# Kernel optimization log

Measured on AMD Instinct MI355X. Metric: run time of the kernel, lower is better.

The kernel has to match this reference:

```python
import jax, jax.numpy as jnp
import numpy as np

B, C, T = 512, 256, 256
E, K, G = 8, 5, 8
EPS = 1e-5


def setup_inputs() -> dict:
    key = jax.random.key(0)
    k1, k2, k3, k4 = jax.random.split(key, 4)
    x = jax.random.normal(k1, (B, C, T), dtype=jnp.float32)
    use_expert_i = jax.random.randint(k2, (B,), 0, E, dtype=jnp.int32)
    # per-expert Conv1d params: weight [E, Cout, Cin, K], bias [E, Cout]
    W = jax.random.normal(k3, (E, C, C, K), dtype=jnp.float32) * 0.05
    b = jax.random.normal(k4, (E, C), dtype=jnp.float32) * 0.05
    # per-expert GroupNorm affine params (torch default init: gamma=1, beta=0)
    gamma = jnp.ones((E, C), dtype=jnp.float32)
    beta = jnp.zeros((E, C), dtype=jnp.float32)
    return {"x": x, "use_expert_i": use_expert_i, "W": W, "b": b,
            "gamma": gamma, "beta": beta}


def _mish(y):
    return y * jnp.tanh(jax.nn.softplus(y))


def reference(x, use_expert_i, W, b, gamma, beta):
    # Top-1 one-hot routing => weight is exactly 1 for the selected expert, so
    # output[b] = Mish(GroupNorm(Conv1d_{e_b}(x[b]))). Gather per-sample params
    # instead of looping over experts (same math, vectorized).
    pad = K // 2
    Wb = W[use_expert_i]        # [B, Cout, Cin, K]
    bb = b[use_expert_i]        # [B, Cout]
    gb = gamma[use_expert_i]    # [B, Cout]
    betab = beta[use_expert_i]  # [B, Cout]

    def per_sample_conv(xi, wi, bi):
        # xi: [Cin, T], wi: [Cout, Cin, K] -> [Cout, T] ('same' padding)
        y = jax.lax.conv_general_dilated(xi[None], wi, window_strides=(1,),
                                         padding=[(pad, pad)])[0]
        return y + bi[:, None]

    y = jax.vmap(per_sample_conv)(x, Wb, bb)  # [B, C, T]

    # GroupNorm: normalize over (channels-in-group, length) per sample
    yg = y.reshape(B, G, C // G, T)
    mu = jnp.mean(yg, axis=(2, 3), keepdims=True)
    var = jnp.var(yg, axis=(2, 3), keepdims=True)
    yn = ((yg - mu) * jax.lax.rsqrt(var + EPS)).reshape(B, C, T)
    yn = yn * gb[:, :, None] + betab[:, :, None]
    return _mish(yn)
```

## Files before the change

### kernel.cpp

```cpp
#include <hip/hip_runtime.h>
#include <cmath>

constexpr int Bn = 512, Cn = 256, Tn = 256, En = 8;
constexpr float EPSf = 1e-5f;

using bf16x8 = __attribute__((ext_vector_type(8))) short;
using f32x4  = __attribute__((ext_vector_type(4))) float;

__device__ __forceinline__ ushort f2bf(float f) {
    uint u = __builtin_bit_cast(uint, f);
    uint r = u + 0x7FFFu + ((u >> 16) & 1u);
    return (ushort)(r >> 16);
}

__global__ __launch_bounds__(256)
void wconv_kernel(const float* __restrict__ Wf, ushort* __restrict__ Wws) {
    int idx = blockIdx.x * 256 + threadIdx.x;
    int ci = idx & 255, co = (idx >> 8) & 255, e = idx >> 16;
    const float* src = Wf + (size_t)idx * 5;
#pragma unroll
    for (int k = 0; k < 5; ++k)
        Wws[(((size_t)(e * 5 + k) * 256 + co) << 8) + ci] = f2bf(src[k]);
}

template<bool USE_WS>
__global__ __launch_bounds__(256)
void conv_mfma(const float* __restrict__ x, const int* __restrict__ expert,
               const float* __restrict__ Wf, const ushort* __restrict__ Wws,
               const float* __restrict__ bias, const float* __restrict__ gamma,
               const float* __restrict__ beta, float* __restrict__ out) {
    int id = blockIdx.x;
    int wg = (id & 7) * 256 + (id >> 3);
    int b  = wg >> 2;
    int gp = wg & 3;
    int e  = __builtin_amdgcn_readfirstlane(expert[b]);
    const int cb = gp * 64;

    const int tid = threadIdx.x;
    const int w = tid >> 6, l = tid & 63, q = l >> 4, r = l & 15;

    __shared__ ushort xT[260 * 40];
    __shared__ float red[4][4];

    f32x4 acc[4][4];
#pragma unroll
    for (int m = 0; m < 4; ++m)
#pragma unroll
        for (int n = 0; n < 4; ++n) acc[m][n] = f32x4{0.f, 0.f, 0.f, 0.f};

    if (tid < 4) {
        int row = (tid < 2) ? tid : (256 + tid);
#pragma unroll
        for (int i = 0; i < 10; ++i)
            *reinterpret_cast<uint2*>(&xT[row * 40 + i * 4]) = make_uint2(0u, 0u);
    }

    for (int ci0 = 0; ci0 < Cn; ci0 += 32) {
        __syncthreads();
        const float* xb = x + ((size_t)b * Cn + ci0 + w * 8) * Tn;
#pragma unroll
        for (int tt = 0; tt < 4; ++tt) {
            const int t = tt * 64 + l;
            float v[8];
#pragma unroll
            for (int rr = 0; rr < 8; ++rr) v[rr] = xb[rr * Tn + t];
            uint p0 = (uint)f2bf(v[0]) | ((uint)f2bf(v[1]) << 16);
            uint p1 = (uint)f2bf(v[2]) | ((uint)f2bf(v[3]) << 16);
            uint p2 = (uint)f2bf(v[4]) | ((uint)f2bf(v[5]) << 16);
            uint p3 = (uint)f2bf(v[6]) | ((uint)f2bf(v[7]) << 16);
            *reinterpret_cast<uint2*>(&xT[(t + 2) * 40 + w * 8])     = make_uint2(p0, p1);
            *reinterpret_cast<uint2*>(&xT[(t + 2) * 40 + w * 8 + 4]) = make_uint2(p2, p3);
        }
        __syncthreads();

#pragma unroll
        for (int k = 0; k < 5; ++k) {
            bf16x8 A[4];
#pragma unroll
            for (int m = 0; m < 4; ++m) {
                if (USE_WS) {
                    A[m] = *reinterpret_cast<const bf16x8*>(
                        Wws + (((size_t)((e * 5 + k) * 256 + cb + m * 16 + r)) << 8)
                            + ci0 + q * 8);
                } else {
                    bf16x8 a;
#pragma unroll
                    for (int j = 0; j < 8; ++j)
                        a[j] = (short)f2bf(
                            Wf[((size_t)((e * 256 + cb + m * 16 + r)) * 256
                                + ci0 + q * 8 + j) * 5 + k]);
                    A[m] = a;
                }
            }
#pragma unroll
            for (int n = 0; n < 4; ++n) {
                const bf16x8 Bf = *reinterpret_cast<const bf16x8*>(
                    &xT[(w * 64 + n * 16 + r + k) * 40 + q * 8]);
#pragma unroll
                for (int m = 0; m < 4; ++m)
                    acc[m][n] = __builtin_amdgcn_mfma_f32_16x16x32_bf16(
                        A[m], Bf, acc[m][n], 0, 0, 0);
            }
        }
    }

    float s1a = 0.f, s2a = 0.f, s1b = 0.f, s2b = 0.f;
#pragma unroll
    for (int m = 0; m < 4; ++m) {
#pragma unroll
        for (int i = 0; i < 4; ++i) {
            const float bv = bias[e * 256 + cb + m * 16 + q * 4 + i];
#pragma unroll
            for (int n = 0; n < 4; ++n) {
                const float v = acc[m][n][i] + bv;
                acc[m][n][i] = v;
                if (m < 2) { s1a += v; s2a += v * v; }
                else       { s1b += v; s2b += v * v; }
            }
        }
    }
#pragma unroll
    for (int off = 32; off; off >>= 1) {
        s1a += __shfl_xor(s1a, off); s2a += __shfl_xor(s2a, off);
        s1b += __shfl_xor(s1b, off); s2b += __shfl_xor(s2b, off);
    }
    if (l == 0) { red[w][0] = s1a; red[w][1] = s2a; red[w][2] = s1b; red[w][3] = s2b; }
    __syncthreads();
    const float S1a = red[0][0] + red[1][0] + red[2][0] + red[3][0];
    const float S2a = red[0][1] + red[1][1] + red[2][1] + red[3][1];
    const float S1b = red[0][2] + red[1][2] + red[2][2] + red[3][2];
    const float S2b = red[0][3] + red[1][3] + red[2][3] + red[3][3];

    constexpr float invn = 1.0f / (32 * 256);
    const float mua = S1a * invn, mub = S1b * invn;
    const float rsa = rsqrtf(fmaf(-mua, mua, S2a * invn) + EPSf);
    const float rsb = rsqrtf(fmaf(-mub, mub, S2b * invn) + EPSf);

#pragma unroll
    for (int m = 0; m < 4; ++m) {
        const float mu = (m < 2) ? mua : mub;
        const float rs = (m < 2) ? rsa : rsb;
#pragma unroll
        for (int i = 0; i < 4; ++i) {
            const int co = cb + m * 16 + q * 4 + i;
            const float sc = gamma[e * 256 + co] * rs;
            const float sh = beta[e * 256 + co] - mu * sc;
            float* orow = out + ((size_t)(b * 256 + co)) * 256 + w * 64 + r;
#pragma unroll
            for (int n = 0; n < 4; ++n) {
                const float y = fmaf(acc[m][n][i], sc, sh);
                const float u  = __expf(y);
                const float t2 = u * (u + 2.f);
                const float ms = (y > 20.f) ? y : y * t2 / (t2 + 2.f);
                orow[n * 16] = ms;
            }
        }
    }
}

extern "C" void kernel_launch(void* const* d_in, const int* in_sizes, int n_in,
                              void* d_out, int out_size, void* d_ws, size_t ws_size,
                              hipStream_t stream) {
    const float* x      = (const float*)d_in[0];
    const int*   expert = (const int*)  d_in[1];
    const float* Wf     = (const float*)d_in[2];
    const float* bias   = (const float*)d_in[3];
    const float* gamma  = (const float*)d_in[4];
    const float* beta   = (const float*)d_in[5];
    float* out = (float*)d_out;

    const size_t W_BYTES = (size_t)En * 5 * 256 * 256 * 2;
    if (ws_size >= W_BYTES) {
        ushort* Wws = (ushort*)d_ws;
        hipLaunchKernelGGL(wconv_kernel, dim3(2048), dim3(256), 0, stream, Wf, Wws);
        hipLaunchKernelGGL((conv_mfma<true>), dim3(2048), dim3(256), 0, stream,
                           x, expert, Wf, Wws, bias, gamma, beta, out);
    } else {
        hipLaunchKernelGGL((conv_mfma<false>), dim3(2048), dim3(256), 0, stream,
                           x, expert, Wf, nullptr, bias, gamma, beta, out);
    }
}
```

Before: 228.3 us.

## Process one full sample per block with 512 threads and prefetched x staging

Each block now computes all 256 output channels for one sample with 8 waves arranged 4x2, instead of four blocks per sample each doing 64 channels. This means the input tile is loaded and converted to bf16 once per sample rather than four times. The next input chunk's global loads are issued into registers before the current chunk's MFMAs, then written to LDS after a barrier, so load latency overlaps compute. In exchange, accumulators double to 128 floats per thread, which raises register pressure under the 512-thread launch bound, and the grid shrinks to 512 blocks.

```diff
diff --git a/kernel.cpp b/kernel.cpp
--- a/kernel.cpp
+++ b/kernel.cpp
@@ -24,29 +24,26 @@
 }
 
 template<bool USE_WS>
-__global__ __launch_bounds__(256)
+__global__ __launch_bounds__(512, 2)
 void conv_mfma(const float* __restrict__ x, const int* __restrict__ expert,
                const float* __restrict__ Wf, const ushort* __restrict__ Wws,
                const float* __restrict__ bias, const float* __restrict__ gamma,
                const float* __restrict__ beta, float* __restrict__ out) {
-    int id = blockIdx.x;
-    int wg = (id & 7) * 256 + (id >> 3);
-    int b  = wg >> 2;
-    int gp = wg & 3;
-    int e  = __builtin_amdgcn_readfirstlane(expert[b]);
-    const int cb = gp * 64;
+    const int b = blockIdx.x;
+    const int e = __builtin_amdgcn_readfirstlane(expert[b]);
 
     const int tid = threadIdx.x;
     const int w = tid >> 6, l = tid & 63, q = l >> 4, r = l & 15;
+    const int wm = w >> 1, wn = w & 1;
 
     __shared__ ushort xT[260 * 40];
-    __shared__ float red[4][4];
+    __shared__ float red[8][4];
 
-    f32x4 acc[4][4];
+    f32x4 acc[4][8];
 #pragma unroll
     for (int m = 0; m < 4; ++m)
 #pragma unroll
-        for (int n = 0; n < 4; ++n) acc[m][n] = f32x4{0.f, 0.f, 0.f, 0.f};
+        for (int n = 0; n < 8; ++n) acc[m][n] = f32x4{0.f, 0.f, 0.f, 0.f};
 
     if (tid < 4) {
         int row = (tid < 2) ? tid : (256 + tid);
@@ -55,23 +52,37 @@
             *reinterpret_cast<uint2*>(&xT[row * 40 + i * 4]) = make_uint2(0u, 0u);
     }
 
-    for (int ci0 = 0; ci0 < Cn; ci0 += 32) {
-        __syncthreads();
-        const float* xb = x + ((size_t)b * Cn + ci0 + w * 8) * Tn;
-#pragma unroll
-        for (int tt = 0; tt < 4; ++tt) {
-            const int t = tt * 64 + l;
-            float v[8];
-#pragma unroll
-            for (int rr = 0; rr < 8; ++rr) v[rr] = xb[rr * Tn + t];
-            uint p0 = (uint)f2bf(v[0]) | ((uint)f2bf(v[1]) << 16);
-            uint p1 = (uint)f2bf(v[2]) | ((uint)f2bf(v[3]) << 16);
-            uint p2 = (uint)f2bf(v[4]) | ((uint)f2bf(v[5]) << 16);
-            uint p3 = (uint)f2bf(v[6]) | ((uint)f2bf(v[7]) << 16);
-            *reinterpret_cast<uint2*>(&xT[(t + 2) * 40 + w * 8])     = make_uint2(p0, p1);
-            *reinterpret_cast<uint2*>(&xT[(t + 2) * 40 + w * 8 + 4]) = make_uint2(p2, p3);
-        }
-        __syncthreads();
+    float v[4][4];
+
+#define STAGE_LOAD(CI0) {                                                   \
+        const float* xb = x + ((size_t)b * Cn + (CI0) + w * 4) * Tn;        \
+        _Pragma("unroll")                                                   \
+        for (int tt = 0; tt < 4; ++tt) {                                    \
+            const int t = tt * 64 + l;                                      \
+            _Pragma("unroll")                                               \
+            for (int rr = 0; rr < 4; ++rr) v[tt][rr] = xb[rr * Tn + t];     \
+        }                                                                   \
+    }
+#define STAGE_WRITE() {                                                     \
+        _Pragma("unroll")                                                   \
+        for (int tt = 0; tt < 4; ++tt) {                                    \
+            const int t = tt * 64 + l;                                      \
+            uint p0 = (uint)f2bf(v[tt][0]) | ((uint)f2bf(v[tt][1]) << 16);  \
+            uint p1 = (uint)f2bf(v[tt][2]) | ((uint)f2bf(v[tt][3]) << 16);  \
+            *reinterpret_cast<uint2*>(&xT[(t + 2) * 40 + w * 4]) =          \
+                make_uint2(p0, p1);                                         \
+        }                                                                   \
+    }
+
+    STAGE_LOAD(0);
+    __syncthreads();
+    STAGE_WRITE();
+    __syncthreads();
+
+#pragma unroll 1
+    for (int ct = 0; ct < 8; ++ct) {
+        const int ci0 = ct * 32;
+        if (ct < 7) STAGE_LOAD(ci0 + 32);
 
 #pragma unroll
         for (int k = 0; k < 5; ++k) {
@@ -80,42 +91,47 @@
             for (int m = 0; m < 4; ++m) {
                 if (USE_WS) {
                     A[m] = *reinterpret_cast<const bf16x8*>(
-                        Wws + (((size_t)((e * 5 + k) * 256 + cb + m * 16 + r)) << 8)
+                        Wws + (((size_t)((e * 5 + k) * 256 + wm * 64 + m * 16 + r)) << 8)
                             + ci0 + q * 8);
                 } else {
                     bf16x8 a;
 #pragma unroll
                     for (int j = 0; j < 8; ++j)
                         a[j] = (short)f2bf(
-                            Wf[((size_t)((e * 256 + cb + m * 16 + r)) * 256
+                            Wf[((size_t)((e * 256 + wm * 64 + m * 16 + r)) * 256
                                 + ci0 + q * 8 + j) * 5 + k]);
                     A[m] = a;
                 }
             }
 #pragma unroll
-            for (int n = 0; n < 4; ++n) {
+            for (int n = 0; n < 8; ++n) {
                 const bf16x8 Bf = *reinterpret_cast<const bf16x8*>(
-                    &xT[(w * 64 + n * 16 + r + k) * 40 + q * 8]);
+                    &xT[(wn * 128 + n * 16 + r + k) * 40 + q * 8]);
 #pragma unroll
                 for (int m = 0; m < 4; ++m)
                     acc[m][n] = __builtin_amdgcn_mfma_f32_16x16x32_bf16(
                         A[m], Bf, acc[m][n], 0, 0, 0);
             }
         }
+        __syncthreads();
+        if (ct < 7) STAGE_WRITE();
+        __syncthreads();
     }
+#undef STAGE_LOAD
+#undef STAGE_WRITE
 
     float s1a = 0.f, s2a = 0.f, s1b = 0.f, s2b = 0.f;
 #pragma unroll
     for (int m = 0; m < 4; ++m) {
 #pragma unroll
         for (int i = 0; i < 4; ++i) {
-            const float bv = bias[e * 256 + cb + m * 16 + q * 4 + i];
+            const float bv = bias[e * Cn + wm * 64 + m * 16 + q * 4 + i];
 #pragma unroll
-            for (int n = 0; n < 4; ++n) {
-                const float v = acc[m][n][i] + bv;
-                acc[m][n][i] = v;
-                if (m < 2) { s1a += v; s2a += v * v; }
-                else       { s1b += v; s2b += v * v; }
+            for (int n = 0; n < 8; ++n) {
+                const float vv = acc[m][n][i] + bv;
+                acc[m][n][i] = vv;
+                if (m < 2) { s1a += vv; s2a += vv * vv; }
+                else       { s1b += vv; s2b += vv * vv; }
             }
         }
     }
@@ -126,10 +142,10 @@
     }
     if (l == 0) { red[w][0] = s1a; red[w][1] = s2a; red[w][2] = s1b; red[w][3] = s2b; }
     __syncthreads();
-    const float S1a = red[0][0] + red[1][0] + red[2][0] + red[3][0];
-    const float S2a = red[0][1] + red[1][1] + red[2][1] + red[3][1];
-    const float S1b = red[0][2] + red[1][2] + red[2][2] + red[3][2];
-    const float S2b = red[0][3] + red[1][3] + red[2][3] + red[3][3];
+    const float S1a = red[wm * 2][0] + red[wm * 2 + 1][0];
+    const float S2a = red[wm * 2][1] + red[wm * 2 + 1][1];
+    const float S1b = red[wm * 2][2] + red[wm * 2 + 1][2];
+    const float S2b = red[wm * 2][3] + red[wm * 2 + 1][3];
 
     constexpr float invn = 1.0f / (32 * 256);
     const float mua = S1a * invn, mub = S1b * invn;
@@ -142,12 +158,12 @@
         const float rs = (m < 2) ? rsa : rsb;
 #pragma unroll
         for (int i = 0; i < 4; ++i) {
-            const int co = cb + m * 16 + q * 4 + i;
-            const float sc = gamma[e * 256 + co] * rs;
-            const float sh = beta[e * 256 + co] - mu * sc;
-            float* orow = out + ((size_t)(b * 256 + co)) * 256 + w * 64 + r;
+            const int co = wm * 64 + m * 16 + q * 4 + i;
+            const float sc = gamma[e * Cn + co] * rs;
+            const float sh = beta[e * Cn + co] - mu * sc;
+            float* orow = out + ((size_t)(b * Cn + co)) * Tn + wn * 128 + r;
 #pragma unroll
-            for (int n = 0; n < 4; ++n) {
+            for (int n = 0; n < 8; ++n) {
                 const float y = fmaf(acc[m][n][i], sc, sh);
                 const float u  = __expf(y);
                 const float t2 = u * (u + 2.f);
@@ -173,10 +189,10 @@
     if (ws_size >= W_BYTES) {
         ushort* Wws = (ushort*)d_ws;
         hipLaunchKernelGGL(wconv_kernel, dim3(2048), dim3(256), 0, stream, Wf, Wws);
-        hipLaunchKernelGGL((conv_mfma<true>), dim3(2048), dim3(256), 0, stream,
+        hipLaunchKernelGGL((conv_mfma<true>), dim3(Bn), dim3(512), 0, stream,
                            x, expert, Wf, Wws, bias, gamma, beta, out);
     } else {
-        hipLaunchKernelGGL((conv_mfma<false>), dim3(2048), dim3(256), 0, stream,
+        hipLaunchKernelGGL((conv_mfma<false>), dim3(Bn), dim3(512), 0, stream,
                            x, expert, Wf, nullptr, bias, gamma, beta, out);
     }
 }
```

After: 225.2 us. No clear change (-1.4%).

## Split conv from GroupNorm/Mish and tile conv blocks by time quarter

Applied to the files above, without the earlier changes.

Conv blocks now cover all output channels for one quarter of the time axis instead of a quarter of the channels over all time. x is therefore read about once per sample plus a halo, and the next input chunk is prefetched into registers during the MFMA loop. GroupNorm statistics are written as per-block partial sums, reduced in a small kernel, and applied with Mish in a separate elementwise kernel. This adds an intermediate y buffer (bf16 when workspace allows) that is written and reread, plus extra launches and precision loss from the bf16 intermediate.

```diff
diff --git a/kernel.cpp b/kernel.cpp
--- a/kernel.cpp
+++ b/kernel.cpp
@@ -12,35 +12,37 @@
     uint r = u + 0x7FFFu + ((u >> 16) & 1u);
     return (ushort)(r >> 16);
 }
+__device__ __forceinline__ float bf2f(ushort u) {
+    uint v = (uint)u << 16;
+    return __builtin_bit_cast(float, v);
+}
 
 __global__ __launch_bounds__(256)
 void wconv_kernel(const float* __restrict__ Wf, ushort* __restrict__ Wws) {
     int idx = blockIdx.x * 256 + threadIdx.x;
+    const float* src = Wf + (size_t)idx * 5;
     int ci = idx & 255, co = (idx >> 8) & 255, e = idx >> 16;
-    const float* src = Wf + (size_t)idx * 5;
 #pragma unroll
     for (int k = 0; k < 5; ++k)
         Wws[(((size_t)(e * 5 + k) * 256 + co) << 8) + ci] = f2bf(src[k]);
 }
 
-template<bool USE_WS>
-__global__ __launch_bounds__(256)
+template<bool YBF16, bool WS_W>
+__global__ __launch_bounds__(256, 4)
 void conv_mfma(const float* __restrict__ x, const int* __restrict__ expert,
                const float* __restrict__ Wf, const ushort* __restrict__ Wws,
-               const float* __restrict__ bias, const float* __restrict__ gamma,
-               const float* __restrict__ beta, float* __restrict__ out) {
-    int id = blockIdx.x;
-    int wg = (id & 7) * 256 + (id >> 3);
-    int b  = wg >> 2;
-    int gp = wg & 3;
-    int e  = __builtin_amdgcn_readfirstlane(expert[b]);
-    const int cb = gp * 64;
-
+               const float* __restrict__ bias,
+               float* __restrict__ partial,
+               void* __restrict__ yout)
+{
+    const int id = blockIdx.x;
+    const int b  = id >> 2, tq = id & 3;
+    const int tb = tq * 64;
+    const int e  = __builtin_amdgcn_readfirstlane(expert[b]);
     const int tid = threadIdx.x;
     const int w = tid >> 6, l = tid & 63, q = l >> 4, r = l & 15;
 
-    __shared__ ushort xT[260 * 40];
-    __shared__ float red[4][4];
+    __shared__ ushort xT[68 * 40];
 
     f32x4 acc[4][4];
 #pragma unroll
@@ -48,46 +50,60 @@
 #pragma unroll
         for (int n = 0; n < 4; ++n) acc[m][n] = f32x4{0.f, 0.f, 0.f, 0.f};
 
-    if (tid < 4) {
-        int row = (tid < 2) ? tid : (256 + tid);
-#pragma unroll
-        for (int i = 0; i < 10; ++i)
-            *reinterpret_cast<uint2*>(&xT[row * 40 + i * 4]) = make_uint2(0u, 0u);
-    }
-
-    for (int ci0 = 0; ci0 < Cn; ci0 += 32) {
-        __syncthreads();
-        const float* xb = x + ((size_t)b * Cn + ci0 + w * 8) * Tn;
-#pragma unroll
-        for (int tt = 0; tt < 4; ++tt) {
-            const int t = tt * 64 + l;
-            float v[8];
-#pragma unroll
-            for (int rr = 0; rr < 8; ++rr) v[rr] = xb[rr * Tn + t];
-            uint p0 = (uint)f2bf(v[0]) | ((uint)f2bf(v[1]) << 16);
-            uint p1 = (uint)f2bf(v[2]) | ((uint)f2bf(v[3]) << 16);
-            uint p2 = (uint)f2bf(v[4]) | ((uint)f2bf(v[5]) << 16);
-            uint p3 = (uint)f2bf(v[6]) | ((uint)f2bf(v[7]) << 16);
-            *reinterpret_cast<uint2*>(&xT[(t + 2) * 40 + w * 8])     = make_uint2(p0, p1);
-            *reinterpret_cast<uint2*>(&xT[(t + 2) * 40 + w * 8 + 4]) = make_uint2(p2, p3);
-        }
-        __syncthreads();
+    const int t1 = tb - 2 + l;
+    const bool ok1 = (t1 >= 0) && (t1 < Tn);
+    const int t2 = tb + 62 + l;
+    const bool ok2 = (l < 4) && (t2 < Tn);
+    float v[8], vh[8];
+
+#define STAGE_LOAD(CI0) {                                                    \
+        const float* xb = x + ((size_t)b * Cn + (CI0) + w * 8) * Tn;         \
+        _Pragma("unroll")                                                    \
+        for (int rr = 0; rr < 8; ++rr) v[rr]  = ok1 ? xb[rr * Tn + t1] : 0.f;\
+        _Pragma("unroll")                                                    \
+        for (int rr = 0; rr < 8; ++rr) vh[rr] = ok2 ? xb[rr * Tn + t2] : 0.f;\
+    }
+#define STAGE_WRITE() {                                                      \
+        uint p0 = (uint)f2bf(v[0]) | ((uint)f2bf(v[1]) << 16);               \
+        uint p1 = (uint)f2bf(v[2]) | ((uint)f2bf(v[3]) << 16);               \
+        uint p2 = (uint)f2bf(v[4]) | ((uint)f2bf(v[5]) << 16);               \
+        uint p3 = (uint)f2bf(v[6]) | ((uint)f2bf(v[7]) << 16);               \
+        *reinterpret_cast<uint2*>(&xT[l * 40 + w * 8])     = make_uint2(p0, p1);\
+        *reinterpret_cast<uint2*>(&xT[l * 40 + w * 8 + 4]) = make_uint2(p2, p3);\
+        if (l < 4) {                                                         \
+            uint h0 = (uint)f2bf(vh[0]) | ((uint)f2bf(vh[1]) << 16);         \
+            uint h1 = (uint)f2bf(vh[2]) | ((uint)f2bf(vh[3]) << 16);         \
+            uint h2 = (uint)f2bf(vh[4]) | ((uint)f2bf(vh[5]) << 16);         \
+            uint h3 = (uint)f2bf(vh[6]) | ((uint)f2bf(vh[7]) << 16);         \
+            *reinterpret_cast<uint2*>(&xT[(64 + l) * 40 + w * 8])     = make_uint2(h0, h1);\
+            *reinterpret_cast<uint2*>(&xT[(64 + l) * 40 + w * 8 + 4]) = make_uint2(h2, h3);\
+        }                                                                    \
+    }
+
+    STAGE_LOAD(0);
+    STAGE_WRITE();
+    __syncthreads();
+
+#pragma unroll 1
+    for (int ct = 0; ct < 8; ++ct) {
+        const int ci0 = ct * 32;
+        if (ct < 7) STAGE_LOAD(ci0 + 32);
 
 #pragma unroll
         for (int k = 0; k < 5; ++k) {
             bf16x8 A[4];
 #pragma unroll
             for (int m = 0; m < 4; ++m) {
-                if (USE_WS) {
+                if (WS_W) {
                     A[m] = *reinterpret_cast<const bf16x8*>(
-                        Wws + (((size_t)((e * 5 + k) * 256 + cb + m * 16 + r)) << 8)
+                        Wws + (((size_t)((e * 5 + k) * 256 + w * 64 + m * 16 + r)) << 8)
                             + ci0 + q * 8);
                 } else {
                     bf16x8 a;
 #pragma unroll
                     for (int j = 0; j < 8; ++j)
                         a[j] = (short)f2bf(
-                            Wf[((size_t)((e * 256 + cb + m * 16 + r)) * 256
+                            Wf[((size_t)(e * 256 + w * 64 + m * 16 + r) * 256
                                 + ci0 + q * 8 + j) * 5 + k]);
                     A[m] = a;
                 }
@@ -95,67 +111,121 @@
 #pragma unroll
             for (int n = 0; n < 4; ++n) {
                 const bf16x8 Bf = *reinterpret_cast<const bf16x8*>(
-                    &xT[(w * 64 + n * 16 + r + k) * 40 + q * 8]);
+                    &xT[(n * 16 + r + k) * 40 + q * 8]);
 #pragma unroll
                 for (int m = 0; m < 4; ++m)
                     acc[m][n] = __builtin_amdgcn_mfma_f32_16x16x32_bf16(
                         A[m], Bf, acc[m][n], 0, 0, 0);
             }
         }
-    }
-
-    float s1a = 0.f, s2a = 0.f, s1b = 0.f, s2b = 0.f;
+        __syncthreads();
+        if (ct < 7) STAGE_WRITE();
+        __syncthreads();
+    }
+#undef STAGE_LOAD
+#undef STAGE_WRITE
+
+    float s1[2] = {0.f, 0.f}, s2[2] = {0.f, 0.f};
 #pragma unroll
     for (int m = 0; m < 4; ++m) {
+        const int gi = m >> 1;
 #pragma unroll
         for (int i = 0; i < 4; ++i) {
-            const float bv = bias[e * 256 + cb + m * 16 + q * 4 + i];
+            const float bv = bias[e * Cn + w * 64 + m * 16 + q * 4 + i];
 #pragma unroll
             for (int n = 0; n < 4; ++n) {
-                const float v = acc[m][n][i] + bv;
-                acc[m][n][i] = v;
-                if (m < 2) { s1a += v; s2a += v * v; }
-                else       { s1b += v; s2b += v * v; }
+                const float val = acc[m][n][i] + bv;
+                acc[m][n][i] = val;
+                s1[gi] += val;
+                s2[gi] += val * val;
             }
         }
     }
 #pragma unroll
     for (int off = 32; off; off >>= 1) {
-        s1a += __shfl_xor(s1a, off); s2a += __shfl_xor(s2a, off);
-        s1b += __shfl_xor(s1b, off); s2b += __shfl_xor(s2b, off);
-    }
-    if (l == 0) { red[w][0] = s1a; red[w][1] = s2a; red[w][2] = s1b; red[w][3] = s2b; }
-    __syncthreads();
-    const float S1a = red[0][0] + red[1][0] + red[2][0] + red[3][0];
-    const float S2a = red[0][1] + red[1][1] + red[2][1] + red[3][1];
-    const float S1b = red[0][2] + red[1][2] + red[2][2] + red[3][2];
-    const float S2b = red[0][3] + red[1][3] + red[2][3] + red[3][3];
-
+        s1[0] += __shfl_xor(s1[0], off); s2[0] += __shfl_xor(s2[0], off);
+        s1[1] += __shfl_xor(s1[1], off); s2[1] += __shfl_xor(s2[1], off);
+    }
+    if (l == 0) {
+        float* p = partial + ((size_t)(b * 4 + tq) * 8 + w * 2) * 2;
+        p[0] = s1[0]; p[1] = s2[0]; p[2] = s1[1]; p[3] = s2[1];
+    }
+
+#pragma unroll
+    for (int m = 0; m < 4; ++m) {
+#pragma unroll
+        for (int i = 0; i < 4; ++i) {
+            const int co = w * 64 + m * 16 + q * 4 + i;
+            const size_t base = ((size_t)(b * Cn + co)) * Tn + tb + r;
+#pragma unroll
+            for (int n = 0; n < 4; ++n) {
+                if (YBF16)
+                    ((ushort*)yout)[base + n * 16] = f2bf(acc[m][n][i]);
+                else
+                    ((float*)yout)[base + n * 16] = acc[m][n][i];
+            }
+        }
+    }
+}
+
+__global__ __launch_bounds__(256)
+void stats_reduce(const float* __restrict__ partial, float* __restrict__ stats) {
+    const int t = blockIdx.x * 256 + threadIdx.x;
+    const int b = t >> 3, g = t & 7;
+    float s1 = 0.f, s2 = 0.f;
+#pragma unroll
+    for (int tq = 0; tq < 4; ++tq) {
+        const float* p = partial + ((size_t)(b * 4 + tq) * 8 + g) * 2;
+        s1 += p[0]; s2 += p[1];
+    }
     constexpr float invn = 1.0f / (32 * 256);
-    const float mua = S1a * invn, mub = S1b * invn;
-    const float rsa = rsqrtf(fmaf(-mua, mua, S2a * invn) + EPSf);
-    const float rsb = rsqrtf(fmaf(-mub, mub, S2b * invn) + EPSf);
-
-#pragma unroll
-    for (int m = 0; m < 4; ++m) {
-        const float mu = (m < 2) ? mua : mub;
-        const float rs = (m < 2) ? rsa : rsb;
-#pragma unroll
-        for (int i = 0; i < 4; ++i) {
-            const int co = cb + m * 16 + q * 4 + i;
-            const float sc = gamma[e * 256 + co] * rs;
-            const float sh = beta[e * 256 + co] - mu * sc;
-            float* orow = out + ((size_t)(b * 256 + co)) * 256 + w * 64 + r;
-#pragma unroll
-            for (int n = 0; n < 4; ++n) {
-                const float y = fmaf(acc[m][n][i], sc, sh);
-                const float u  = __expf(y);
-                const float t2 = u * (u + 2.f);
-                const float ms = (y > 20.f) ? y : y * t2 / (t2 + 2.f);
-                orow[n * 16] = ms;
-            }
-        }
-    }
+    const float mu  = s1 * invn;
+    const float var = fmaf(-mu, mu, s2 * invn);
+    stats[t * 2]     = mu;
+    stats[t * 2 + 1] = rsqrtf(var + EPSf);
+}
+
+template<bool YBF16>
+__global__ __launch_bounds__(256)
+void norm_mish(const void* __restrict__ yin, const int* __restrict__ expert,
+               const float* __restrict__ stats,
+               const float* __restrict__ gamma, const float* __restrict__ beta,
+               float* __restrict__ out)
+{
+    const int idx = blockIdx.x * 256 + threadIdx.x;
+    const int row = idx >> 5, seg = idx & 31;
+    const int b = row >> 8, co = row & 255, g = co >> 5;
+    const int e = expert[b];
+    const float mu = stats[(b * 8 + g) * 2];
+    const float rs = stats[(b * 8 + g) * 2 + 1];
+    const float sc = gamma[e * Cn + co] * rs;
+    const float sh = beta[e * Cn + co] - mu * sc;
+    const size_t base = (size_t)row * Tn + seg * 8;
+
+    float yv[8];
+    if (YBF16) {
+        const bf16x8 raw = *reinterpret_cast<const bf16x8*>((const ushort*)yin + base);
+#pragma unroll
+        for (int j = 0; j < 8; ++j) yv[j] = bf2f((ushort)raw[j]);
+    } else {
+        const float4 a = *reinterpret_cast<const float4*>((const float*)yin + base);
+        const float4 c = *reinterpret_cast<const float4*>((const float*)yin + base + 4);
+        yv[0] = a.x; yv[1] = a.y; yv[2] = a.z; yv[3] = a.w;
+        yv[4] = c.x; yv[5] = c.y; yv[6] = c.z; yv[7] = c.w;
+    }
+
+    float o[8];
+#pragma unroll
+    for (int j = 0; j < 8; ++j) {
+        const float y  = fmaf(yv[j], sc, sh);
+        const float u  = __expf(y);
+        const float t2 = u * (u + 2.f);
+        o[j] = (y > 20.f) ? y : y * t2 / (t2 + 2.f);
+    }
+    float4 o0 = {o[0], o[1], o[2], o[3]};
+    float4 o1 = {o[4], o[5], o[6], o[7]};
+    *reinterpret_cast<float4*>(out + base)     = o0;
+    *reinterpret_cast<float4*>(out + base + 4) = o1;
 }
 
 extern "C" void kernel_launch(void* const* d_in, const int* in_sizes, int n_in,
@@ -169,14 +239,49 @@
     const float* beta   = (const float*)d_in[5];
     float* out = (float*)d_out;
 
-    const size_t W_BYTES = (size_t)En * 5 * 256 * 256 * 2;
-    if (ws_size >= W_BYTES) {
-        ushort* Wws = (ushort*)d_ws;
+    const size_t WWS_BYTES  = (size_t)En * 5 * 256 * 256 * 2;
+    const size_t PART_BYTES = (size_t)Bn * 4 * 8 * 2 * 4;
+    const size_t STAT_BYTES = (size_t)Bn * 8 * 2 * 4;
+    const size_t Y_BYTES    = (size_t)Bn * Cn * Tn * 2;
+
+    const bool ws_w  = ws_size >= WWS_BYTES + PART_BYTES + STAT_BYTES;
+    char* wsb = (char*)d_ws;
+
+    ushort* Wws;
+    float *partial, *stats;
+    if (ws_w) {
+        Wws     = (ushort*)wsb;
+        partial = (float*)(wsb + WWS_BYTES);
+        stats   = (float*)(wsb + WWS_BYTES + PART_BYTES);
+    } else {
+        Wws     = nullptr;
+        partial = (float*)wsb;
+        stats   = (float*)(wsb + PART_BYTES);
+    }
+    const size_t y_off = ws_w ? (WWS_BYTES + PART_BYTES + STAT_BYTES)
+                              : (PART_BYTES + STAT_BYTES);
+    const bool ybf = ws_size >= y_off + Y_BYTES;
+    void* ybuf = ybf ? (void*)(wsb + y_off) : (void*)out;
+
+    if (ws_w)
         hipLaunchKernelGGL(wconv_kernel, dim3(2048), dim3(256), 0, stream, Wf, Wws);
-        hipLaunchKernelGGL((conv_mfma<true>), dim3(2048), dim3(256), 0, stream,
-                           x, expert, Wf, Wws, bias, gamma, beta, out);
-    } else {
-        hipLaunchKernelGGL((conv_mfma<false>), dim3(2048), dim3(256), 0, stream,
-                           x, expert, Wf, nullptr, bias, gamma, beta, out);
-    }
-}
+
+    if (ws_w && ybf)
+        hipLaunchKernelGGL((conv_mfma<true, true>), dim3(2048), dim3(256), 0, stream,
+                           x, expert, Wf, Wws, bias, partial, ybuf);
+    else if (ws_w)
+        hipLaunchKernelGGL((conv_mfma<false, true>), dim3(2048), dim3(256), 0, stream,
+                           x, expert, Wf, Wws, bias, partial, ybuf);
+    else
+        hipLaunchKernelGGL((conv_mfma<false, false>), dim3(2048), dim3(256), 0, stream,
+                           x, expert, Wf, nullptr, bias, partial, ybuf);
+
+    hipLaunchKernelGGL(stats_reduce, dim3(16), dim3(256), 0, stream, partial, stats);
+
+    if (ybf)
+        hipLaunchKernelGGL((norm_mish<true>), dim3(16384), dim3(256), 0, stream,
+                           ybuf, expert, stats, gamma, beta, out);
+    else
+        hipLaunchKernelGGL((norm_mish<false>), dim3(16384), dim3(256), 0, stream,
+                           ybuf, expert, stats, gamma, beta, out);
+}
```

Measured after the change: 334.9 us. 46.7% more time.

## Double-buffer x tile in LDS with register prefetch and batched weight loads

Applied to the files above, without the earlier changes.

Adds a second LDS buffer for the transposed bf16 x tile. Global loads for chunk ct+2 are issued into registers while chunk ct is computed, and chunk ct+1 is written to the other buffer, so one barrier per iteration replaces two. All 20 weight fragments for a chunk are now loaded before the MFMA loop, and launch bounds request 2 blocks per SM. The cost is much higher register pressure (32 prefetch floats plus 20 bf16x8 fragments on top of 64 accumulators) and doubled LDS, which could cause spills or limit occupancy.

```diff
diff --git a/kernel.cpp b/kernel.cpp
--- a/kernel.cpp
+++ b/kernel.cpp
@@ -16,30 +16,31 @@
 __global__ __launch_bounds__(256)
 void wconv_kernel(const float* __restrict__ Wf, ushort* __restrict__ Wws) {
     int idx = blockIdx.x * 256 + threadIdx.x;
+    const float* src = Wf + (size_t)idx * 5;
     int ci = idx & 255, co = (idx >> 8) & 255, e = idx >> 16;
-    const float* src = Wf + (size_t)idx * 5;
 #pragma unroll
     for (int k = 0; k < 5; ++k)
         Wws[(((size_t)(e * 5 + k) * 256 + co) << 8) + ci] = f2bf(src[k]);
 }
 
-template<bool USE_WS>
-__global__ __launch_bounds__(256)
-void conv_mfma(const float* __restrict__ x, const int* __restrict__ expert,
-               const float* __restrict__ Wf, const ushort* __restrict__ Wws,
-               const float* __restrict__ bias, const float* __restrict__ gamma,
-               const float* __restrict__ beta, float* __restrict__ out) {
-    int id = blockIdx.x;
-    int wg = (id & 7) * 256 + (id >> 3);
-    int b  = wg >> 2;
-    int gp = wg & 3;
-    int e  = __builtin_amdgcn_readfirstlane(expert[b]);
+template<bool WS_W>
+__global__ __launch_bounds__(256, 2)
+void conv_gn_mish(const float* __restrict__ x, const int* __restrict__ expert,
+                  const float* __restrict__ Wf, const ushort* __restrict__ Wws,
+                  const float* __restrict__ bias, const float* __restrict__ gamma,
+                  const float* __restrict__ beta, float* __restrict__ out)
+{
+    const int id = blockIdx.x;
+    const int wg = (id & 7) * 256 + (id >> 3);
+    const int b  = wg >> 2;
+    const int gp = wg & 3;
     const int cb = gp * 64;
+    const int e  = __builtin_amdgcn_readfirstlane(expert[b]);
 
     const int tid = threadIdx.x;
     const int w = tid >> 6, l = tid & 63, q = l >> 4, r = l & 15;
 
-    __shared__ ushort xT[260 * 40];
+    __shared__ ushort xT[2][260 * 40];
     __shared__ float red[4][4];
 
     f32x4 acc[4][4];
@@ -48,38 +49,60 @@
 #pragma unroll
         for (int n = 0; n < 4; ++n) acc[m][n] = f32x4{0.f, 0.f, 0.f, 0.f};
 
-    if (tid < 4) {
-        int row = (tid < 2) ? tid : (256 + tid);
+    if (tid < 8) {
+        const int bf = tid >> 2, rr = tid & 3;
+        const int row = (rr < 2) ? rr : (256 + rr);
 #pragma unroll
         for (int i = 0; i < 10; ++i)
-            *reinterpret_cast<uint2*>(&xT[row * 40 + i * 4]) = make_uint2(0u, 0u);
-    }
-
-    for (int ci0 = 0; ci0 < Cn; ci0 += 32) {
-        __syncthreads();
-        const float* xb = x + ((size_t)b * Cn + ci0 + w * 8) * Tn;
-#pragma unroll
-        for (int tt = 0; tt < 4; ++tt) {
-            const int t = tt * 64 + l;
-            float v[8];
-#pragma unroll
-            for (int rr = 0; rr < 8; ++rr) v[rr] = xb[rr * Tn + t];
-            uint p0 = (uint)f2bf(v[0]) | ((uint)f2bf(v[1]) << 16);
-            uint p1 = (uint)f2bf(v[2]) | ((uint)f2bf(v[3]) << 16);
-            uint p2 = (uint)f2bf(v[4]) | ((uint)f2bf(v[5]) << 16);
-            uint p3 = (uint)f2bf(v[6]) | ((uint)f2bf(v[7]) << 16);
-            *reinterpret_cast<uint2*>(&xT[(t + 2) * 40 + w * 8])     = make_uint2(p0, p1);
-            *reinterpret_cast<uint2*>(&xT[(t + 2) * 40 + w * 8 + 4]) = make_uint2(p2, p3);
-        }
-        __syncthreads();
-
+            *reinterpret_cast<uint2*>(&xT[bf][row * 40 + i * 4]) = make_uint2(0u, 0u);
+    }
+
+    float v[4][8];
+
+#define STAGE_LOAD(CI0) {                                                    \
+        const float* xb = x + ((size_t)b * Cn + (CI0) + w * 8) * Tn;         \
+        _Pragma("unroll")                                                    \
+        for (int tt = 0; tt < 4; ++tt) {                                     \
+            const int t = tt * 64 + l;                                       \
+            _Pragma("unroll")                                                \
+            for (int rr = 0; rr < 8; ++rr) v[tt][rr] = xb[rr * Tn + t];      \
+        }                                                                    \
+    }
+#define STAGE_WRITE(BUF) {                                                   \
+        ushort* dst = xT[BUF];                                               \
+        _Pragma("unroll")                                                    \
+        for (int tt = 0; tt < 4; ++tt) {                                     \
+            const int t = tt * 64 + l;                                       \
+            uint p0 = (uint)f2bf(v[tt][0]) | ((uint)f2bf(v[tt][1]) << 16);   \
+            uint p1 = (uint)f2bf(v[tt][2]) | ((uint)f2bf(v[tt][3]) << 16);   \
+            uint p2 = (uint)f2bf(v[tt][4]) | ((uint)f2bf(v[tt][5]) << 16);   \
+            uint p3 = (uint)f2bf(v[tt][6]) | ((uint)f2bf(v[tt][7]) << 16);   \
+            *reinterpret_cast<uint2*>(&dst[(t + 2) * 40 + w * 8])     = make_uint2(p0, p1); \
+            *reinterpret_cast<uint2*>(&dst[(t + 2) * 40 + w * 8 + 4]) = make_uint2(p2, p3); \
+        }                                                                    \
+    }
+
+    STAGE_LOAD(0);
+    STAGE_WRITE(0);
+    STAGE_LOAD(32);
+    __syncthreads();
+
+#pragma unroll 1
+    for (int ct = 0; ct < 8; ++ct) {
+        if (ct < 7) {
+            STAGE_WRITE((ct + 1) & 1);
+            if (ct < 6) STAGE_LOAD((ct + 2) * 32);
+        }
+        const int ci0 = ct * 32;
+        const ushort* src = xT[ct & 1];
+
+        bf16x8 A[5][4];
 #pragma unroll
         for (int k = 0; k < 5; ++k) {
-            bf16x8 A[4];
 #pragma unroll
             for (int m = 0; m < 4; ++m) {
-                if (USE_WS) {
-                    A[m] = *reinterpret_cast<const bf16x8*>(
+                if (WS_W) {
+                    A[k][m] = *reinterpret_cast<const bf16x8*>(
                         Wws + (((size_t)((e * 5 + k) * 256 + cb + m * 16 + r)) << 8)
                             + ci0 + q * 8);
                 } else {
@@ -87,35 +110,41 @@
 #pragma unroll
                     for (int j = 0; j < 8; ++j)
                         a[j] = (short)f2bf(
-                            Wf[((size_t)((e * 256 + cb + m * 16 + r)) * 256
+                            Wf[((size_t)(e * 256 + cb + m * 16 + r) * 256
                                 + ci0 + q * 8 + j) * 5 + k]);
-                    A[m] = a;
+                    A[k][m] = a;
                 }
             }
+        }
+#pragma unroll
+        for (int k = 0; k < 5; ++k) {
 #pragma unroll
             for (int n = 0; n < 4; ++n) {
                 const bf16x8 Bf = *reinterpret_cast<const bf16x8*>(
-                    &xT[(w * 64 + n * 16 + r + k) * 40 + q * 8]);
+                    &src[(w * 64 + n * 16 + r + k) * 40 + q * 8]);
 #pragma unroll
                 for (int m = 0; m < 4; ++m)
                     acc[m][n] = __builtin_amdgcn_mfma_f32_16x16x32_bf16(
-                        A[m], Bf, acc[m][n], 0, 0, 0);
-            }
-        }
-    }
+                        A[k][m], Bf, acc[m][n], 0, 0, 0);
+            }
+        }
+        __syncthreads();
+    }
+#undef STAGE_LOAD
+#undef STAGE_WRITE
 
     float s1a = 0.f, s2a = 0.f, s1b = 0.f, s2b = 0.f;
 #pragma unroll
     for (int m = 0; m < 4; ++m) {
 #pragma unroll
         for (int i = 0; i < 4; ++i) {
-            const float bv = bias[e * 256 + cb + m * 16 + q * 4 + i];
+            const float bv = bias[e * Cn + cb + m * 16 + q * 4 + i];
 #pragma unroll
             for (int n = 0; n < 4; ++n) {
-                const float v = acc[m][n][i] + bv;
-                acc[m][n][i] = v;
-                if (m < 2) { s1a += v; s2a += v * v; }
-                else       { s1b += v; s2b += v * v; }
+                const float val = acc[m][n][i] + bv;
+                acc[m][n][i] = val;
+                if (m < 2) { s1a += val; s2a += val * val; }
+                else       { s1b += val; s2b += val * val; }
             }
         }
     }
@@ -143,9 +172,9 @@
 #pragma unroll
         for (int i = 0; i < 4; ++i) {
             const int co = cb + m * 16 + q * 4 + i;
-            const float sc = gamma[e * 256 + co] * rs;
-            const float sh = beta[e * 256 + co] - mu * sc;
-            float* orow = out + ((size_t)(b * 256 + co)) * 256 + w * 64 + r;
+            const float sc = gamma[e * Cn + co] * rs;
+            const float sh = beta[e * Cn + co] - mu * sc;
+            float* orow = out + ((size_t)(b * Cn + co)) * Tn + w * 64 + r;
 #pragma unroll
             for (int n = 0; n < 4; ++n) {
                 const float y = fmaf(acc[m][n][i], sc, sh);
@@ -169,14 +198,15 @@
     const float* beta   = (const float*)d_in[5];
     float* out = (float*)d_out;
 
-    const size_t W_BYTES = (size_t)En * 5 * 256 * 256 * 2;
-    if (ws_size >= W_BYTES) {
+    const size_t WWS_BYTES = (size_t)En * 5 * 256 * 256 * 2;
+
+    if (ws_size >= WWS_BYTES) {
         ushort* Wws = (ushort*)d_ws;
         hipLaunchKernelGGL(wconv_kernel, dim3(2048), dim3(256), 0, stream, Wf, Wws);
-        hipLaunchKernelGGL((conv_mfma<true>), dim3(2048), dim3(256), 0, stream,
+        hipLaunchKernelGGL((conv_gn_mish<true>), dim3(2048), dim3(256), 0, stream,
                            x, expert, Wf, Wws, bias, gamma, beta, out);
     } else {
-        hipLaunchKernelGGL((conv_mfma<false>), dim3(2048), dim3(256), 0, stream,
+        hipLaunchKernelGGL((conv_gn_mish<false>), dim3(2048), dim3(256), 0, stream,
                            x, expert, Wf, nullptr, bias, gamma, beta, out);
     }
 }
```

Result: faster. 218.2 us (-4.4%).
